# Optimization experiments

Measured on AMD Instinct MI355X. Metric: run time of the kernel, lower is better.

The kernel has to match this reference:

```python
import jax, jax.numpy as jnp
import numpy as np

H_MAX = 0.05
TIME_LEN = 5  # t = linspace(0, 1, 5); uniform segments of length 0.25
N_STEPS = int(np.ceil(0.25 / H_MAX))  # Euler steps per segment = 5 (matches torch ode_solve)


def setup_inputs() -> dict:
    key = jax.random.key(0)
    k1, k2, k3, k4, k5 = jax.random.split(key, 5)
    bs, d, hidden = 1024, 1024, 2048
    z0 = jax.random.normal(k1, (bs, d), dtype=jnp.float32)
    t = jnp.linspace(0.0, 1.0, TIME_LEN).astype(jnp.float32)
    # MLP ODEF params: f(z, t) = tanh([z, t] @ W1 + b1) @ W2 + b2
    s1 = 1.0 / np.sqrt(d + 1)
    s2 = 1.0 / np.sqrt(hidden)
    W1 = jax.random.uniform(k2, (d + 1, hidden), jnp.float32, -s1, s1)
    b1 = jax.random.uniform(k3, (hidden,), jnp.float32, -s1, s1)
    W2 = jax.random.uniform(k4, (hidden, d), jnp.float32, -s2, s2)
    b2 = jax.random.uniform(k5, (d,), jnp.float32, -s2, s2)
    return {"z0": z0, "t": t, "W1": W1, "b1": b1, "W2": W2, "b2": b2}


def _f(z, t_scalar, W1, b1, W2, b2):
    # z: [bs, d]; t_scalar broadcast as an extra input feature
    bs = z.shape[0]
    zt = jnp.concatenate([z, jnp.full((bs, 1), t_scalar, dtype=z.dtype)], axis=1)
    h = jnp.tanh(zt @ W1 + b1)
    return h @ W2 + b2


def _ode_solve(z0, t0, t1, W1, b1, W2, b2):
    # Euler: z <- z + h * f(z, t), N_STEPS fixed steps (h_max = 0.05)
    h = (t1 - t0) / N_STEPS

    def step(carry, _):
        z, t = carry
        z = z + h * _f(z, t, W1, b1, W2, b2)
        return (z, t + h), None

    (z, _), _ = jax.lax.scan(step, (z0, t0), None, length=N_STEPS)
    return z


def reference(z0, t, W1, b1, W2, b2):
    # NeuralODE.forward with return_whole_sequence=False: returns z at final time point.
    z = z0
    for i in range(TIME_LEN - 1):  # small fixed loop over time checkpoints
        z = _ode_solve(z, t[i], t[i + 1], W1, b1, W2, b2)
    return z
```

## Files before the change

### kernel.cpp

```cpp
#include <hip/hip_runtime.h>
#include <cstdint>
#include <cstddef>


typedef __bf16 bf16x8 __attribute__((ext_vector_type(8)));
typedef float f32x4 __attribute__((ext_vector_type(4)));

#define WAITV(N) asm volatile("s_waitcnt vmcnt(" #N ") lgkmcnt(0)" ::: "memory")
#define BARRIER() asm volatile("s_barrier" ::: "memory")

__device__ __forceinline__ unsigned short f2bf(float f) {
  union { float f; unsigned u; } v; v.f = f;
  unsigned r = v.u + 0x7fffu + ((v.u >> 16) & 1u);
  return (unsigned short)(r >> 16);
}

__device__ __forceinline__ float fast_tanh(float x) {
  float e = __builtin_amdgcn_exp2f(x * 2.8853900817779268f);
  return 1.0f - 2.0f * __builtin_amdgcn_rcpf(1.0f + e);
}

__global__ void transpose_to_bf16(const float* __restrict__ in,
                                  unsigned short* __restrict__ out,
                                  int rows, int cols) {
  __shared__ float tile[32][33];
  int c0 = blockIdx.x * 32, r0 = blockIdx.y * 32;
  int tx = threadIdx.x, ty = threadIdx.y;
#pragma unroll
  for (int j = 0; j < 32; j += 8)
    tile[ty + j][tx] = in[(size_t)(r0 + ty + j) * cols + (c0 + tx)];
  __syncthreads();
#pragma unroll
  for (int j = 0; j < 32; j += 8)
    out[(size_t)(c0 + ty + j) * rows + (r0 + tx)] = f2bf(tile[tx][ty + j]);
}

__global__ void prep_misc(const float* __restrict__ z0,
                          float* __restrict__ zf,
                          unsigned short* __restrict__ zbf,
                          const float* __restrict__ W1,
                          float* __restrict__ w1l, int n, int nl) {
  int i = blockIdx.x * blockDim.x + threadIdx.x;
  if (i < n) { float v = z0[i]; zf[i] = v; zbf[i] = f2bf(v); }
  if (i < nl) { w1l[i] = W1[(size_t)1024 * 2048 + i]; }
}

__device__ __forceinline__ void stage64(const unsigned short* __restrict__ g,
                                        size_t ld, int row0, int k0,
                                        unsigned short* lds, int tid) {
  int r = tid >> 3;
  int c = (tid & 7) ^ (r & 7);
  __builtin_amdgcn_global_load_lds(
      (const __attribute__((address_space(1))) void*)(
          g + (size_t)(row0 + r) * ld + k0 + c * 8),
      (__attribute__((address_space(3))) void*)(lds + tid * 8), 16, 0, 0);
}

__device__ __forceinline__ bf16x8 frag_ld(const unsigned short* lds, int row,
                                          int chunk_logical, int x) {
  return *(const bf16x8*)(lds + row * 64 + ((chunk_logical ^ x) << 3));
}

__global__ __launch_bounds__(512, 1) void gemm1_kernel(
    const unsigned short* __restrict__ Zb,
    const unsigned short* __restrict__ W1T,
    unsigned short* __restrict__ H,
    const float* __restrict__ b1, const float* __restrict__ w1l, float tval) {
  __shared__ __align__(16) unsigned short lds[24576];
  const int tid = threadIdx.x;
  const int lane = tid & 63, wid = tid >> 6;
  const int l15 = lane & 15, q = lane >> 4, x = l15 & 7;
  const int bid = blockIdx.x;
  const int xcd = bid & 7, loc = bid >> 3;
  const int mt = (loc & 3) | ((xcd & 3) << 2);
  const int nt = (loc >> 2) | ((xcd >> 2) << 3);
  const int m0 = mt * 64, n0 = nt * 128;

  f32x4 acc[2][2] = {};

  auto stage_tile = [&](int t, int b) {
    int k = t * 64;
    unsigned short* p = lds + b * 12288;
    stage64(Zb, 1024, m0, k, p, tid);
    stage64(W1T, 1024, n0, k, p + 4096, tid);
    stage64(W1T, 1024, n0 + 64, k, p + 8192, tid);
  };
  auto compute = [&](int b) {
    const unsigned short* A = lds + b * 12288 + (wid & 1) * 2048;
    const unsigned short* B = lds + b * 12288 + 4096 + (wid >> 1) * 2048;
#pragma unroll
    for (int kk = 0; kk < 2; ++kk) {
      bf16x8 a[2], bb[2];
#pragma unroll
      for (int im = 0; im < 2; ++im)
        a[im] = frag_ld(A, im * 16 + l15, (kk << 2) + q, x);
#pragma unroll
      for (int jn = 0; jn < 2; ++jn)
        bb[jn] = frag_ld(B, jn * 16 + l15, (kk << 2) + q, x);
#pragma unroll
      for (int im = 0; im < 2; ++im)
#pragma unroll
        for (int jn = 0; jn < 2; ++jn)
          acc[im][jn] = __builtin_amdgcn_mfma_f32_16x16x32_bf16(
              a[im], bb[jn], acc[im][jn], 0, 0, 0);
    }
  };

  stage_tile(0, 0);
  stage_tile(1, 1);
  for (int i = 0; i < 15; ++i) {
    WAITV(3);
    BARRIER();
    compute(i & 1);
    if (i < 14) {
      BARRIER();
      stage_tile(i + 2, i & 1);
    }
  }
  WAITV(0);
  BARRIER();
  compute(1);

#pragma unroll
  for (int jn = 0; jn < 2; ++jn) {
    int col = n0 + (wid >> 1) * 32 + jn * 16 + l15;
    float bb = b1[col] + tval * w1l[col];
#pragma unroll
    for (int im = 0; im < 2; ++im) {
      int rowb = m0 + (wid & 1) * 32 + im * 16 + q * 4;
#pragma unroll
      for (int r = 0; r < 4; ++r)
        H[(size_t)(rowb + r) * 2048 + col] =
            f2bf(fast_tanh(acc[im][jn][r] + bb));
    }
  }
}

__global__ __launch_bounds__(512, 1) void gemm2_kernel(
    const unsigned short* __restrict__ Hb,
    const unsigned short* __restrict__ W2T,
    const float* __restrict__ b2,
    const float* __restrict__ zf,
    float* __restrict__ outf,
    unsigned short* __restrict__ zbf,
    float h) {
  __shared__ __align__(16) unsigned short lds[32768];
  const int tid = threadIdx.x;
  const int lane = tid & 63, wid = tid >> 6;
  const int l15 = lane & 15, q = lane >> 4, x = l15 & 7;
  const int kh = wid >> 2, mh = (wid >> 1) & 1, nh = wid & 1;
  const int bid = blockIdx.x;
  const int xcd = bid & 7, loc = bid >> 3;
  const int mt = (loc & 3) | ((xcd & 3) << 2);
  const int nt = (loc >> 2) | ((xcd >> 2) << 3);
  const int m0 = mt * 64, n0 = nt * 64;

  f32x4 acc[2][2] = {};

  auto stage_tile = [&](int t, int b) {
    int k = t * 64;
    unsigned short* p = lds + b * 16384;
    stage64(Hb, 2048, m0, k, p, tid);
    stage64(Hb, 2048, m0, k + 1024, p + 4096, tid);
    stage64(W2T, 2048, n0, k, p + 8192, tid);
    stage64(W2T, 2048, n0, k + 1024, p + 12288, tid);
  };
  auto compute = [&](int b) {
    const unsigned short* A = lds + b * 16384 + kh * 4096 + mh * 2048;
    const unsigned short* B = lds + b * 16384 + 8192 + kh * 4096 + nh * 2048;
#pragma unroll
    for (int kk = 0; kk < 2; ++kk) {
      bf16x8 a[2], bb[2];
#pragma unroll
      for (int im = 0; im < 2; ++im)
        a[im] = frag_ld(A, im * 16 + l15, (kk << 2) + q, x);
#pragma unroll
      for (int jn = 0; jn < 2; ++jn)
        bb[jn] = frag_ld(B, jn * 16 + l15, (kk << 2) + q, x);
#pragma unroll
      for (int im = 0; im < 2; ++im)
#pragma unroll
        for (int jn = 0; jn < 2; ++jn)
          acc[im][jn] = __builtin_amdgcn_mfma_f32_16x16x32_bf16(
              a[im], bb[jn], acc[im][jn], 0, 0, 0);
    }
  };

  stage_tile(0, 0);
  stage_tile(1, 1);
  for (int i = 0; i < 15; ++i) {
    WAITV(4);
    BARRIER();
    compute(i & 1);
    if (i < 14) {
      BARRIER();
      stage_tile(i + 2, i & 1);
    }
  }
  WAITV(0);
  BARRIER();
  compute(1);

  __syncthreads();
  float* red = (float*)lds;
  const int region = (mh * 2 + nh) * 1056;
  if (kh == 1) {
#pragma unroll
    for (int im = 0; im < 2; ++im)
#pragma unroll
      for (int jn = 0; jn < 2; ++jn) {
        int c = jn * 16 + l15;
#pragma unroll
        for (int r = 0; r < 4; ++r)
          red[region + (im * 16 + q * 4 + r) * 33 + c] = acc[im][jn][r];
      }
  }
  __syncthreads();
  if (kh == 0) {
#pragma unroll
    for (int jn = 0; jn < 2; ++jn) {
      int coll = nh * 32 + jn * 16 + l15;
      int col = n0 + coll;
      float bb = b2[col];
#pragma unroll
      for (int im = 0; im < 2; ++im) {
        int rowl = im * 16 + q * 4;
#pragma unroll
        for (int r = 0; r < 4; ++r) {
          float s = acc[im][jn][r] +
                    red[region + (rowl + r) * 33 + jn * 16 + l15];
          size_t gidx = (size_t)(m0 + mh * 32 + rowl + r) * 1024 + col;
          float zv = zf[gidx] + h * (s + bb);
          outf[gidx] = zv;
          zbf[gidx] = f2bf(zv);
        }
      }
    }
  }
}

extern "C" void kernel_launch(void* const* d_in, const int* in_sizes, int n_in,
                              void* d_out, int out_size, void* d_ws,
                              size_t ws_size, hipStream_t stream) {
  const float* z0 = (const float*)d_in[0];
  const float* W1 = (const float*)d_in[2];
  const float* b1 = (const float*)d_in[3];
  const float* W2 = (const float*)d_in[4];
  const float* b2 = (const float*)d_in[5];
  float* out = (float*)d_out;

  char* ws = (char*)d_ws;
  unsigned short* W1T = (unsigned short*)(ws + 0);
  unsigned short* W2T = (unsigned short*)(ws + (4u << 20));
  unsigned short* zbf = (unsigned short*)(ws + (8u << 20));
  unsigned short* Hbf = (unsigned short*)(ws + (10u << 20));
  float* zf = (float*)(ws + (14u << 20));
  float* w1l = (float*)(ws + (18u << 20));

  transpose_to_bf16<<<dim3(64, 32), dim3(32, 8), 0, stream>>>(W1, W1T, 1024, 2048);
  transpose_to_bf16<<<dim3(32, 64), dim3(32, 8), 0, stream>>>(W2, W2T, 2048, 1024);
  prep_misc<<<4096, 256, 0, stream>>>(z0, zf, zbf, W1, w1l, 1024 * 1024, 2048);

  const float h = 0.05f;
  for (int seg = 0; seg < 4; ++seg) {
    float tcur = 0.25f * (float)seg;
    for (int j = 0; j < 5; ++j) {
      gemm1_kernel<<<256, 512, 0, stream>>>(zbf, W1T, Hbf, b1, w1l, tcur);
      bool last = (seg == 3 && j == 4);
      float* outf = last ? out : zf;
      gemm2_kernel<<<256, 512, 0, stream>>>(Hbf, W2T, b2, zf, outf, zbf, h);
      tcur += h;
    }
  }
}
```

Before: 458.8 us.

## Load A fragments directly to registers and deepen B LDS pipeline to four stages

In both GEMM kernels the A operand is now loaded straight from global memory into registers, double-buffered across iterations, instead of being staged through LDS. Only the weight (B) tiles go through LDS, now in a four-deep ring buffer with a single barrier per k-step rather than two. The aim is to cut LDS traffic and barrier stalls and to hide more global-load latency. The cost is more register pressure, uncoalesced-ish per-lane A loads, and a fixed vmcnt(6) wait that may not cover the tail iterations correctly.

Measured after the change: 989.5 us. 2.16x slower.

```diff
diff --git a/kernel.cpp b/kernel.cpp
--- a/kernel.cpp
+++ b/kernel.cpp
@@ -66,7 +66,7 @@
     const unsigned short* __restrict__ W1T,
     unsigned short* __restrict__ H,
     const float* __restrict__ b1, const float* __restrict__ w1l, float tval) {
-  __shared__ __align__(16) unsigned short lds[24576];
+  __shared__ __align__(16) unsigned short lds[32768];
   const int tid = threadIdx.x;
   const int lane = tid & 63, wid = tid >> 6;
   const int l15 = lane & 15, q = lane >> 4, x = l15 & 7;
@@ -75,59 +75,73 @@
   const int mt = (loc & 3) | ((xcd & 3) << 2);
   const int nt = (loc >> 2) | ((xcd >> 2) << 3);
   const int m0 = mt * 64, n0 = nt * 128;
+  const int wm = (wid & 1) * 32, wn = (wid >> 1) * 32;
+
+  const unsigned short* gA = Zb + (size_t)(m0 + wm + l15) * 1024 + q * 8;
 
   f32x4 acc[2][2] = {};
-
-  auto stage_tile = [&](int t, int b) {
+  bf16x8 a0r[2][2], a1r[2][2];
+
+  auto stageB = [&](int t, int b) {
     int k = t * 64;
-    unsigned short* p = lds + b * 12288;
-    stage64(Zb, 1024, m0, k, p, tid);
-    stage64(W1T, 1024, n0, k, p + 4096, tid);
-    stage64(W1T, 1024, n0 + 64, k, p + 8192, tid);
-  };
-  auto compute = [&](int b) {
-    const unsigned short* A = lds + b * 12288 + (wid & 1) * 2048;
-    const unsigned short* B = lds + b * 12288 + 4096 + (wid >> 1) * 2048;
+    unsigned short* p = lds + b * 8192;
+    stage64(W1T, 1024, n0, k, p, tid);
+    stage64(W1T, 1024, n0 + 64, k, p + 4096, tid);
+  };
+  auto loadA = [&](int t, bf16x8 dst[2][2]) {
+    int k = t * 64;
+#pragma unroll
+    for (int kk = 0; kk < 2; ++kk)
+#pragma unroll
+      for (int im = 0; im < 2; ++im)
+        dst[kk][im] =
+            *(const bf16x8*)(gA + (size_t)(im * 16) * 1024 + k + kk * 32);
+  };
+  auto compute = [&](int b, bf16x8 (&ar)[2][2]) {
+    const unsigned short* B = lds + b * 8192;
 #pragma unroll
     for (int kk = 0; kk < 2; ++kk) {
-      bf16x8 a[2], bb[2];
-#pragma unroll
-      for (int im = 0; im < 2; ++im)
-        a[im] = frag_ld(A, im * 16 + l15, (kk << 2) + q, x);
+      bf16x8 bb[2];
 #pragma unroll
       for (int jn = 0; jn < 2; ++jn)
-        bb[jn] = frag_ld(B, jn * 16 + l15, (kk << 2) + q, x);
+        bb[jn] = frag_ld(B, wn + jn * 16 + l15, (kk << 2) + q, x);
 #pragma unroll
       for (int im = 0; im < 2; ++im)
 #pragma unroll
         for (int jn = 0; jn < 2; ++jn)
           acc[im][jn] = __builtin_amdgcn_mfma_f32_16x16x32_bf16(
-              a[im], bb[jn], acc[im][jn], 0, 0, 0);
-    }
-  };
-
-  stage_tile(0, 0);
-  stage_tile(1, 1);
-  for (int i = 0; i < 15; ++i) {
-    WAITV(3);
+              ar[kk][im], bb[jn], acc[im][jn], 0, 0, 0);
+    }
+  };
+
+  stageB(0, 0);
+  stageB(1, 1);
+  stageB(2, 2);
+  loadA(0, a0r);
+#pragma unroll 1
+  for (int i = 0; i < 16; i += 2) {
+    WAITV(6);
     BARRIER();
-    compute(i & 1);
-    if (i < 14) {
-      BARRIER();
-      stage_tile(i + 2, i & 1);
-    }
-  }
-  WAITV(0);
-  BARRIER();
-  compute(1);
+    if (i < 15) loadA(i + 1, a1r);
+    __builtin_amdgcn_sched_barrier(0);
+    if (i < 13) stageB(i + 3, (i + 3) & 3);
+    compute(i & 3, a0r);
+
+    WAITV(6);
+    BARRIER();
+    if (i + 1 < 15) loadA(i + 2, a0r);
+    __builtin_amdgcn_sched_barrier(0);
+    if (i + 1 < 13) stageB(i + 4, (i + 4) & 3);
+    compute((i + 1) & 3, a1r);
+  }
 
 #pragma unroll
   for (int jn = 0; jn < 2; ++jn) {
-    int col = n0 + (wid >> 1) * 32 + jn * 16 + l15;
+    int col = n0 + wn + jn * 16 + l15;
     float bb = b1[col] + tval * w1l[col];
 #pragma unroll
     for (int im = 0; im < 2; ++im) {
-      int rowb = m0 + (wid & 1) * 32 + im * 16 + q * 4;
+      int rowb = m0 + wm + im * 16 + q * 4;
 #pragma unroll
       for (int r = 0; r < 4; ++r)
         H[(size_t)(rowb + r) * 2048 + col] =
@@ -155,51 +169,64 @@
   const int nt = (loc >> 2) | ((xcd >> 2) << 3);
   const int m0 = mt * 64, n0 = nt * 64;
 
+  const unsigned short* gA =
+      Hb + (size_t)(m0 + mh * 32 + l15) * 2048 + kh * 1024 + q * 8;
+
   f32x4 acc[2][2] = {};
-
-  auto stage_tile = [&](int t, int b) {
+  bf16x8 a0r[2][2], a1r[2][2];
+
+  auto stageB = [&](int t, int b) {
     int k = t * 64;
-    unsigned short* p = lds + b * 16384;
-    stage64(Hb, 2048, m0, k, p, tid);
-    stage64(Hb, 2048, m0, k + 1024, p + 4096, tid);
-    stage64(W2T, 2048, n0, k, p + 8192, tid);
-    stage64(W2T, 2048, n0, k + 1024, p + 12288, tid);
-  };
-  auto compute = [&](int b) {
-    const unsigned short* A = lds + b * 16384 + kh * 4096 + mh * 2048;
-    const unsigned short* B = lds + b * 16384 + 8192 + kh * 4096 + nh * 2048;
+    unsigned short* p = lds + b * 8192;
+    stage64(W2T, 2048, n0, k, p, tid);
+    stage64(W2T, 2048, n0, k + 1024, p + 4096, tid);
+  };
+  auto loadA = [&](int t, bf16x8 dst[2][2]) {
+    int k = t * 64;
+#pragma unroll
+    for (int kk = 0; kk < 2; ++kk)
+#pragma unroll
+      for (int im = 0; im < 2; ++im)
+        dst[kk][im] =
+            *(const bf16x8*)(gA + (size_t)(im * 16) * 2048 + k + kk * 32);
+  };
+  auto compute = [&](int b, bf16x8 (&ar)[2][2]) {
+    const unsigned short* B = lds + b * 8192 + kh * 4096;
 #pragma unroll
     for (int kk = 0; kk < 2; ++kk) {
-      bf16x8 a[2], bb[2];
-#pragma unroll
-      for (int im = 0; im < 2; ++im)
-        a[im] = frag_ld(A, im * 16 + l15, (kk << 2) + q, x);
+      bf16x8 bb[2];
 #pragma unroll
       for (int jn = 0; jn < 2; ++jn)
-        bb[jn] = frag_ld(B, jn * 16 + l15, (kk << 2) + q, x);
+        bb[jn] = frag_ld(B, nh * 32 + jn * 16 + l15, (kk << 2) + q, x);
 #pragma unroll
       for (int im = 0; im < 2; ++im)
 #pragma unroll
         for (int jn = 0; jn < 2; ++jn)
           acc[im][jn] = __builtin_amdgcn_mfma_f32_16x16x32_bf16(
-              a[im], bb[jn], acc[im][jn], 0, 0, 0);
-    }
-  };
-
-  stage_tile(0, 0);
-  stage_tile(1, 1);
-  for (int i = 0; i < 15; ++i) {
-    WAITV(4);
+              ar[kk][im], bb[jn], acc[im][jn], 0, 0, 0);
+    }
+  };
+
+  stageB(0, 0);
+  stageB(1, 1);
+  stageB(2, 2);
+  loadA(0, a0r);
+#pragma unroll 1
+  for (int i = 0; i < 16; i += 2) {
+    WAITV(6);
     BARRIER();
-    compute(i & 1);
-    if (i < 14) {
-      BARRIER();
-      stage_tile(i + 2, i & 1);
-    }
-  }
-  WAITV(0);
-  BARRIER();
-  compute(1);
+    if (i < 15) loadA(i + 1, a1r);
+    __builtin_amdgcn_sched_barrier(0);
+    if (i < 13) stageB(i + 3, (i + 3) & 3);
+    compute(i & 3, a0r);
+
+    WAITV(6);
+    BARRIER();
+    if (i + 1 < 15) loadA(i + 2, a0r);
+    __builtin_amdgcn_sched_barrier(0);
+    if (i + 1 < 13) stageB(i + 4, (i + 4) & 3);
+    compute((i + 1) & 3, a1r);
+  }
 
   __syncthreads();
   float* red = (float*)lds;
```

## Switch GEMMs to 32x32x16 MFMA with 2-wave blocks and larger per-wave tiles

Applied to the files above, without the earlier changes.

Both GEMM kernels move from 16x16x32 to 32x32x16 bf16 MFMA, shrink blocks from 8 waves to 2 waves (128 threads), and give each wave a 64x64 output tile. LDS staging becomes 16-row chunks with a new XOR swizzle that matches the 32-row fragment reads. The aim is higher MFMA efficiency and fewer LDS fragment loads per flop. The cost is only 2 waves per CU with the same 256-block grid, so latency hiding and occupancy drop sharply.

New measurement: 928.9 us. 102% more time.

```diff
diff --git a/kernel.cpp b/kernel.cpp
--- a/kernel.cpp
+++ b/kernel.cpp
@@ -4,7 +4,7 @@
 
 
 typedef __bf16 bf16x8 __attribute__((ext_vector_type(8)));
-typedef float f32x4 __attribute__((ext_vector_type(4)));
+typedef float f32x16 __attribute__((ext_vector_type(16)));
 
 #define WAITV(N) asm volatile("s_waitcnt vmcnt(" #N ") lgkmcnt(0)" ::: "memory")
 #define BARRIER() asm volatile("s_barrier" ::: "memory")
@@ -45,23 +45,28 @@
   if (i < nl) { w1l[i] = W1[(size_t)1024 * 2048 + i]; }
 }
 
-__device__ __forceinline__ void stage64(const unsigned short* __restrict__ g,
-                                        size_t ld, int row0, int k0,
-                                        unsigned short* lds, int tid) {
-  int r = tid >> 3;
-  int c = (tid & 7) ^ (r & 7);
+__device__ __forceinline__ int swz(int r) { return (r ^ (r >> 3)) & 7; }
+
+__device__ __forceinline__ void stage16(const unsigned short* __restrict__ g,
+                                        size_t ld, int grow0, int k0,
+                                        unsigned short* region, int lrow0,
+                                        int tid) {
+  int rr = tid >> 3;
+  int rl = lrow0 + rr;
+  int c = (tid & 7) ^ swz(rl);
   __builtin_amdgcn_global_load_lds(
       (const __attribute__((address_space(1))) void*)(
-          g + (size_t)(row0 + r) * ld + k0 + c * 8),
-      (__attribute__((address_space(3))) void*)(lds + tid * 8), 16, 0, 0);
-}
-
-__device__ __forceinline__ bf16x8 frag_ld(const unsigned short* lds, int row,
-                                          int chunk_logical, int x) {
-  return *(const bf16x8*)(lds + row * 64 + ((chunk_logical ^ x) << 3));
-}
-
-__global__ __launch_bounds__(512, 1) void gemm1_kernel(
+          g + (size_t)(grow0 + rr) * ld + k0 + c * 8),
+      (__attribute__((address_space(3))) void*)(region + lrow0 * 64 + tid * 8),
+      16, 0, 0);
+}
+
+__device__ __forceinline__ bf16x8 frag64(const unsigned short* region, int row,
+                                         int c) {
+  return *(const bf16x8*)(region + row * 64 + ((c ^ swz(row)) << 3));
+}
+
+__global__ __launch_bounds__(128) void gemm1_kernel(
     const unsigned short* __restrict__ Zb,
     const unsigned short* __restrict__ W1T,
     unsigned short* __restrict__ H,
@@ -69,47 +74,52 @@
   __shared__ __align__(16) unsigned short lds[24576];
   const int tid = threadIdx.x;
   const int lane = tid & 63, wid = tid >> 6;
-  const int l15 = lane & 15, q = lane >> 4, x = l15 & 7;
+  const int l31 = lane & 31, h5 = lane >> 5;
   const int bid = blockIdx.x;
   const int xcd = bid & 7, loc = bid >> 3;
   const int mt = (loc & 3) | ((xcd & 3) << 2);
   const int nt = (loc >> 2) | ((xcd >> 2) << 3);
   const int m0 = mt * 64, n0 = nt * 128;
 
-  f32x4 acc[2][2] = {};
+  f32x16 acc[2][2] = {};
 
   auto stage_tile = [&](int t, int b) {
     int k = t * 64;
-    unsigned short* p = lds + b * 12288;
-    stage64(Zb, 1024, m0, k, p, tid);
-    stage64(W1T, 1024, n0, k, p + 4096, tid);
-    stage64(W1T, 1024, n0 + 64, k, p + 8192, tid);
+    unsigned short* A = lds + b * 12288;
+    unsigned short* B = lds + b * 12288 + 4096;
+#pragma unroll
+    for (int s = 0; s < 4; ++s)
+      stage16(Zb, 1024, m0 + s * 16, k, A, s * 16, tid);
+#pragma unroll
+    for (int s = 0; s < 8; ++s)
+      stage16(W1T, 1024, n0 + s * 16, k, B, s * 16, tid);
   };
   auto compute = [&](int b) {
-    const unsigned short* A = lds + b * 12288 + (wid & 1) * 2048;
-    const unsigned short* B = lds + b * 12288 + 4096 + (wid >> 1) * 2048;
-#pragma unroll
-    for (int kk = 0; kk < 2; ++kk) {
+    const unsigned short* A = lds + b * 12288;
+    const unsigned short* B = lds + b * 12288 + 4096;
+#pragma unroll
+    for (int ks = 0; ks < 4; ++ks) {
+      int c = ks * 2 + h5;
       bf16x8 a[2], bb[2];
 #pragma unroll
+      for (int im = 0; im < 2; ++im) a[im] = frag64(A, im * 32 + l31, c);
+#pragma unroll
+      for (int jn = 0; jn < 2; ++jn)
+        bb[jn] = frag64(B, wid * 64 + jn * 32 + l31, c);
+#pragma unroll
       for (int im = 0; im < 2; ++im)
-        a[im] = frag_ld(A, im * 16 + l15, (kk << 2) + q, x);
-#pragma unroll
-      for (int jn = 0; jn < 2; ++jn)
-        bb[jn] = frag_ld(B, jn * 16 + l15, (kk << 2) + q, x);
-#pragma unroll
-      for (int im = 0; im < 2; ++im)
 #pragma unroll
         for (int jn = 0; jn < 2; ++jn)
-          acc[im][jn] = __builtin_amdgcn_mfma_f32_16x16x32_bf16(
+          acc[im][jn] = __builtin_amdgcn_mfma_f32_32x32x16_bf16(
               a[im], bb[jn], acc[im][jn], 0, 0, 0);
     }
   };
 
   stage_tile(0, 0);
   stage_tile(1, 1);
+#pragma unroll 1
   for (int i = 0; i < 15; ++i) {
-    WAITV(3);
+    WAITV(12);
     BARRIER();
     compute(i & 1);
     if (i < 14) {
@@ -123,20 +133,21 @@
 
 #pragma unroll
   for (int jn = 0; jn < 2; ++jn) {
-    int col = n0 + (wid >> 1) * 32 + jn * 16 + l15;
+    int col = n0 + wid * 64 + jn * 32 + l31;
     float bb = b1[col] + tval * w1l[col];
 #pragma unroll
     for (int im = 0; im < 2; ++im) {
-      int rowb = m0 + (wid & 1) * 32 + im * 16 + q * 4;
-#pragma unroll
-      for (int r = 0; r < 4; ++r)
-        H[(size_t)(rowb + r) * 2048 + col] =
-            f2bf(fast_tanh(acc[im][jn][r] + bb));
-    }
-  }
-}
-
-__global__ __launch_bounds__(512, 1) void gemm2_kernel(
+      int rowb = m0 + im * 32 + 4 * h5;
+#pragma unroll
+      for (int j = 0; j < 16; ++j) {
+        int row = rowb + (j & 3) + 8 * (j >> 2);
+        H[(size_t)row * 2048 + col] = f2bf(fast_tanh(acc[im][jn][j] + bb));
+      }
+    }
+  }
+}
+
+__global__ __launch_bounds__(128) void gemm2_kernel(
     const unsigned short* __restrict__ Hb,
     const unsigned short* __restrict__ W2T,
     const float* __restrict__ b2,
@@ -146,50 +157,56 @@
     float h) {
   __shared__ __align__(16) unsigned short lds[32768];
   const int tid = threadIdx.x;
-  const int lane = tid & 63, wid = tid >> 6;
-  const int l15 = lane & 15, q = lane >> 4, x = l15 & 7;
-  const int kh = wid >> 2, mh = (wid >> 1) & 1, nh = wid & 1;
+  const int lane = tid & 63, kh = tid >> 6;
+  const int l31 = lane & 31, h5 = lane >> 5;
   const int bid = blockIdx.x;
   const int xcd = bid & 7, loc = bid >> 3;
   const int mt = (loc & 3) | ((xcd & 3) << 2);
   const int nt = (loc >> 2) | ((xcd >> 2) << 3);
   const int m0 = mt * 64, n0 = nt * 64;
 
-  f32x4 acc[2][2] = {};
+  f32x16 acc[2][2] = {};
 
   auto stage_tile = [&](int t, int b) {
     int k = t * 64;
     unsigned short* p = lds + b * 16384;
-    stage64(Hb, 2048, m0, k, p, tid);
-    stage64(Hb, 2048, m0, k + 1024, p + 4096, tid);
-    stage64(W2T, 2048, n0, k, p + 8192, tid);
-    stage64(W2T, 2048, n0, k + 1024, p + 12288, tid);
+#pragma unroll
+    for (int kk = 0; kk < 2; ++kk) {
+      unsigned short* A = p + kk * 4096;
+      unsigned short* B = p + 8192 + kk * 4096;
+#pragma unroll
+      for (int s = 0; s < 4; ++s)
+        stage16(Hb, 2048, m0 + s * 16, k + kk * 1024, A, s * 16, tid);
+#pragma unroll
+      for (int s = 0; s < 4; ++s)
+        stage16(W2T, 2048, n0 + s * 16, k + kk * 1024, B, s * 16, tid);
+    }
   };
   auto compute = [&](int b) {
-    const unsigned short* A = lds + b * 16384 + kh * 4096 + mh * 2048;
-    const unsigned short* B = lds + b * 16384 + 8192 + kh * 4096 + nh * 2048;
-#pragma unroll
-    for (int kk = 0; kk < 2; ++kk) {
+    const unsigned short* A = lds + b * 16384 + kh * 4096;
+    const unsigned short* B = lds + b * 16384 + 8192 + kh * 4096;
+#pragma unroll
+    for (int ks = 0; ks < 4; ++ks) {
+      int c = ks * 2 + h5;
       bf16x8 a[2], bb[2];
 #pragma unroll
+      for (int im = 0; im < 2; ++im) a[im] = frag64(A, im * 32 + l31, c);
+#pragma unroll
+      for (int jn = 0; jn < 2; ++jn) bb[jn] = frag64(B, jn * 32 + l31, c);
+#pragma unroll
       for (int im = 0; im < 2; ++im)
-        a[im] = frag_ld(A, im * 16 + l15, (kk << 2) + q, x);
-#pragma unroll
-      for (int jn = 0; jn < 2; ++jn)
-        bb[jn] = frag_ld(B, jn * 16 + l15, (kk << 2) + q, x);
-#pragma unroll
-      for (int im = 0; im < 2; ++im)
 #pragma unroll
         for (int jn = 0; jn < 2; ++jn)
-          acc[im][jn] = __builtin_amdgcn_mfma_f32_16x16x32_bf16(
+          acc[im][jn] = __builtin_amdgcn_mfma_f32_32x32x16_bf16(
               a[im], bb[jn], acc[im][jn], 0, 0, 0);
     }
   };
 
   stage_tile(0, 0);
   stage_tile(1, 1);
+#pragma unroll 1
   for (int i = 0; i < 15; ++i) {
-    WAITV(4);
+    WAITV(16);
     BARRIER();
     compute(i & 1);
     if (i < 14) {
@@ -203,33 +220,33 @@
 
   __syncthreads();
   float* red = (float*)lds;
-  const int region = (mh * 2 + nh) * 1056;
   if (kh == 1) {
 #pragma unroll
-    for (int im = 0; im < 2; ++im)
+    for (int im = 0; im < 2; ++im) {
+      int rowb = im * 32 + 4 * h5;
 #pragma unroll
       for (int jn = 0; jn < 2; ++jn) {
-        int c = jn * 16 + l15;
-#pragma unroll
-        for (int r = 0; r < 4; ++r)
-          red[region + (im * 16 + q * 4 + r) * 33 + c] = acc[im][jn][r];
+        int col = jn * 32 + l31;
+#pragma unroll
+        for (int j = 0; j < 16; ++j)
+          red[(rowb + (j & 3) + 8 * (j >> 2)) * 65 + col] = acc[im][jn][j];
       }
+    }
   }
   __syncthreads();
   if (kh == 0) {
 #pragma unroll
     for (int jn = 0; jn < 2; ++jn) {
-      int coll = nh * 32 + jn * 16 + l15;
-      int col = n0 + coll;
+      int col = n0 + jn * 32 + l31;
       float bb = b2[col];
 #pragma unroll
       for (int im = 0; im < 2; ++im) {
-        int rowl = im * 16 + q * 4;
-#pragma unroll
-        for (int r = 0; r < 4; ++r) {
-          float s = acc[im][jn][r] +
-                    red[region + (rowl + r) * 33 + jn * 16 + l15];
-          size_t gidx = (size_t)(m0 + mh * 32 + rowl + r) * 1024 + col;
+        int rowb = im * 32 + 4 * h5;
+#pragma unroll
+        for (int j = 0; j < 16; ++j) {
+          int rl = rowb + (j & 3) + 8 * (j >> 2);
+          float s = acc[im][jn][j] + red[rl * 65 + jn * 32 + l31];
+          size_t gidx = (size_t)(m0 + rl) * 1024 + col;
           float zv = zf[gidx] + h * (s + bb);
           outf[gidx] = zv;
           zbf[gidx] = f2bf(zv);
@@ -265,10 +282,10 @@
   for (int seg = 0; seg < 4; ++seg) {
     float tcur = 0.25f * (float)seg;
     for (int j = 0; j < 5; ++j) {
-      gemm1_kernel<<<256, 512, 0, stream>>>(zbf, W1T, Hbf, b1, w1l, tcur);
+      gemm1_kernel<<<256, 128, 0, stream>>>(zbf, W1T, Hbf, b1, w1l, tcur);
       bool last = (seg == 3 && j == 4);
       float* outf = last ? out : zf;
-      gemm2_kernel<<<256, 512, 0, stream>>>(Hbf, W2T, b2, zf, outf, zbf, h);
+      gemm2_kernel<<<256, 128, 0, stream>>>(Hbf, W2T, b2, zf, outf, zbf, h);
       tcur += h;
     }
   }
```
